# Kernel optimization log

Hardware: AMD Instinct MI355X
Metric: run time of the kernel (lower is better)

## Reference

```python
import jax, jax.numpy as jnp
import numpy as np

B, T, N = 512, 512, 128   # batch, timesteps, driving series
M = 64                    # LSTM hidden size
UNITS = 64                # attention units


def setup_inputs() -> dict:
    key = jax.random.key(0)
    ks = jax.random.split(key, 9)
    s = lambda fan_in: 1.0 / np.sqrt(fan_in)
    return {
        "x": jax.random.normal(ks[0], (B, T, N), jnp.float32),
        "hidden_state": jax.random.normal(ks[1], (B, M), jnp.float32),
        "cell_state": jax.random.normal(ks[2], (B, M), jnp.float32),
        # Dense(units) applied to x permuted to (B, N, T): kernel contracts T
        "w1_kernel": jax.random.normal(ks[3], (T, UNITS), jnp.float32) * s(T),
        "w1_bias": jnp.zeros((UNITS,), jnp.float32),
        # Dense(units) applied to query (B, N, 2M)
        "w2_kernel": jax.random.normal(ks[4], (2 * M, UNITS), jnp.float32) * s(2 * M),
        "w2_bias": jnp.zeros((UNITS,), jnp.float32),
        # Dense(1) scoring
        "v_kernel": jax.random.normal(ks[5], (UNITS, 1), jnp.float32) * s(UNITS),
        "v_bias": jnp.zeros((1,), jnp.float32),
    }


def reference(x, hidden_state, cell_state, w1_kernel, w1_bias,
              w2_kernel, w2_bias, v_kernel, v_bias):
    # query: (B, 2M) -> broadcast over the N feature axis (RepeatVector)
    query = jnp.concatenate([hidden_state, cell_state], axis=-1)
    q_proj = query @ w2_kernel + w2_bias                    # (B, UNITS)
    x_perm = jnp.transpose(x, (0, 2, 1))                    # (B, N, T)
    score = jnp.tanh(x_perm @ w1_kernel + w1_bias + q_proj[:, None, :])  # (B, N, UNITS)
    score = score @ v_kernel + v_bias                       # (B, N, 1)
    score = jnp.transpose(score, (0, 2, 1))                 # (B, 1, N)
    attention_weights = jax.nn.softmax(score, axis=-1)      # (B, 1, N)
    context_vector = jnp.sum(attention_weights * x, axis=-1)  # (B, T)
    return context_vector, attention_weights
```

## Files before the change

kernel.cpp:

```cpp
#include <hip/hip_runtime.h>
#include <hip/hip_bf16.h>

namespace {

constexpr int kB = 512, kT = 512, kN = 128, kM = 64, kU = 64;
constexpr int TT = 64;
constexpr int SX = 68;

typedef __attribute__((ext_vector_type(8))) short short8;
typedef __attribute__((ext_vector_type(16))) float f32x16;

__device__ __forceinline__ unsigned pack_hl(float v) {
  unsigned u = __float_as_uint(v);
  unsigned hs = (u + 0x7fffu + ((u >> 16) & 1u)) >> 16;
  float lo = v - __uint_as_float(hs << 16);
  unsigned ul = __float_as_uint(lo);
  unsigned ls = (ul + 0x7fffu + ((ul >> 16) & 1u)) >> 16;
  return (hs << 16) | (ls & 0xffffu);
}

__device__ __forceinline__ float fast_tanh(float x) {
  return 1.0f - 2.0f / (__expf(2.0f * x) + 1.0f);
}

union FragU { unsigned u[4]; short8 s; };

__device__ __forceinline__ void unpack_hl(const unsigned* p, short8& hi, short8& lo) {
  FragU H, L;
#pragma unroll
  for (int j = 0; j < 4; ++j) {
    unsigned a = p[2 * j], b = p[2 * j + 1];
    H.u[j] = (a >> 16) | (b & 0xffff0000u);
    L.u[j] = (a & 0xffffu) | (b << 16);
  }
  hi = H.s; lo = L.s;
}

struct __align__(16) SmemS {
  unsigned xsT[kN * SX];
  unsigned w1T[kU * SX];
  float qpart[8][kU];
  float sred[2][kN];
  float sn[kN];
};

__global__ __launch_bounds__(512, 4) void score_kernel(
    const float* __restrict__ x,
    const float* __restrict__ hs,
    const float* __restrict__ cs,
    const float* __restrict__ w1,
    const float* __restrict__ w1b,
    const float* __restrict__ w2,
    const float* __restrict__ w2b,
    const float* __restrict__ vk,
    float* __restrict__ aw_out)
{
  __shared__ SmemS s;
  const int b = blockIdx.x;
  const int tid = threadIdx.x;
  const int l = tid & 63;
  const int w = tid >> 6;

  {
    const int u = tid & 63, kg = tid >> 6;
    float a0 = 0.f;
#pragma unroll
    for (int j = 0; j < 16; ++j) {
      int k = kg * 16 + j;
      float qv = (k < kM) ? hs[(size_t)b * kM + k] : cs[(size_t)b * kM + (k - kM)];
      a0 = fmaf(qv, w2[k * kU + u], a0);
    }
    s.qpart[kg][u] = a0;
  }

  const int xn = l + 64 * (w & 1);
  const int xts = (w >> 1) * 16;
  const int wu = l;
  const int wts = w * 8;

  const int kh = l >> 5;
  const int mrow = (w & 3) * 32 + (l & 31);
  const int urow = (w >> 2) * 32 + (l & 31);

  f32x16 acc;
#pragma unroll
  for (int i = 0; i < 16; ++i) acc[i] = 0.f;

  float rx[16], rw[8];
#pragma unroll
  for (int j = 0; j < 16; ++j)
    rx[j] = x[((size_t)b * kT + xts + j) * kN + xn];
#pragma unroll
  for (int j = 0; j < 8; ++j)
    rw[j] = w1[(size_t)(wts + j) * kU + wu];

  for (int t0 = 0; t0 < kT; t0 += TT) {
    __syncthreads();
    {
      unsigned px[16];
#pragma unroll
      for (int j = 0; j < 16; ++j) px[j] = pack_hl(rx[j]);
#pragma unroll
      for (int jj = 0; jj < 4; ++jj)
        *(uint4*)&s.xsT[xn * SX + xts + 4 * jj] =
            make_uint4(px[4 * jj], px[4 * jj + 1], px[4 * jj + 2], px[4 * jj + 3]);
      unsigned pw[8];
#pragma unroll
      for (int j = 0; j < 8; ++j) pw[j] = pack_hl(rw[j]);
#pragma unroll
      for (int jj = 0; jj < 2; ++jj)
        *(uint4*)&s.w1T[wu * SX + wts + 4 * jj] =
            make_uint4(pw[4 * jj], pw[4 * jj + 1], pw[4 * jj + 2], pw[4 * jj + 3]);
    }
    __syncthreads();
    if (t0 + TT < kT) {
#pragma unroll
      for (int j = 0; j < 16; ++j)
        rx[j] = x[((size_t)b * kT + t0 + TT + xts + j) * kN + xn];
#pragma unroll
      for (int j = 0; j < 8; ++j)
        rw[j] = w1[(size_t)(t0 + TT + wts + j) * kU + wu];
    }

#pragma unroll
    for (int ss = 0; ss < 4; ++ss) {
      unsigned ra[8];
      const unsigned* pa = &s.xsT[mrow * SX + 16 * ss + 8 * kh];
      *(uint4*)&ra[0] = *(const uint4*)pa;
      *(uint4*)&ra[4] = *(const uint4*)(pa + 4);
      short8 ah, al;
      unpack_hl(ra, ah, al);

      unsigned rb[8];
      const unsigned* pb = &s.w1T[urow * SX + 16 * ss + 8 * kh];
      *(uint4*)&rb[0] = *(const uint4*)pb;
      *(uint4*)&rb[4] = *(const uint4*)(pb + 4);
      short8 bh, bl;
      unpack_hl(rb, bh, bl);

      acc = __builtin_amdgcn_mfma_f32_32x32x16_bf16(ah, bh, acc, 0, 0, 0);
      acc = __builtin_amdgcn_mfma_f32_32x32x16_bf16(ah, bl, acc, 0, 0, 0);
      acc = __builtin_amdgcn_mfma_f32_32x32x16_bf16(al, bh, acc, 0, 0, 0);
    }
  }

  float qpu = w2b[urow] + w1b[urow];
#pragma unroll
  for (int g = 0; g < 8; ++g) qpu += s.qpart[g][urow];
  const float vu = vk[urow];

  float pr[16];
#pragma unroll
  for (int r = 0; r < 16; ++r)
    pr[r] = fast_tanh(acc[r] + qpu) * vu;
#pragma unroll
  for (int off = 1; off < 32; off <<= 1)
#pragma unroll
    for (int r = 0; r < 16; ++r)
      pr[r] += __shfl_xor(pr[r], off);

  if ((l & 31) == 0) {
#pragma unroll
    for (int r = 0; r < 16; ++r)
      s.sred[w >> 2][(w & 3) * 32 + (r & 3) + 8 * (r >> 2) + 4 * kh] = pr[r];
  }
  __syncthreads();
  if (tid < kN) s.sn[tid] = s.sred[0][tid] + s.sred[1][tid];
  __syncthreads();

  if (tid < 64) {
    float s0 = s.sn[tid], s1 = s.sn[tid + 64];
    float m = fmaxf(s0, s1);
#pragma unroll
    for (int off = 32; off > 0; off >>= 1) m = fmaxf(m, __shfl_xor(m, off));
    float e0 = __expf(s0 - m), e1 = __expf(s1 - m);
    float se = e0 + e1;
#pragma unroll
    for (int off = 32; off > 0; off >>= 1) se += __shfl_xor(se, off);
    float inv = 1.0f / se;
    aw_out[(size_t)b * kN + tid] = e0 * inv;
    aw_out[(size_t)b * kN + tid + 64] = e1 * inv;
  }
}

__global__ __launch_bounds__(256) void context_kernel(
    const float* __restrict__ x,
    const float* __restrict__ aw_in,
    float* __restrict__ ctx)
{
  __shared__ float aw[kN];
  const int b = blockIdx.x >> 2;
  const int seg = blockIdx.x & 3;
  if (threadIdx.x < kN) aw[threadIdx.x] = aw_in[(size_t)b * kN + threadIdx.x];
  __syncthreads();

  const int lr = threadIdx.x & 3;
  const int row = threadIdx.x >> 2;
#pragma unroll
  for (int rg = 0; rg < 2; ++rg) {
    const int r = seg * 128 + rg * 64 + row;
    const float4* xp = (const float4*)(x + ((size_t)b * kT + r) * kN);
    float a = 0.f;
#pragma unroll
    for (int k = 0; k < 8; ++k) {
      int i = lr + k * 4;
      float4 v = xp[i];
      const float* wa = &aw[i * 4];
      a = fmaf(v.x, wa[0], a);
      a = fmaf(v.y, wa[1], a);
      a = fmaf(v.z, wa[2], a);
      a = fmaf(v.w, wa[3], a);
    }
    a += __shfl_xor(a, 1);
    a += __shfl_xor(a, 2);
    if (lr == 0) ctx[(size_t)b * kT + r] = a;
  }
}

}

extern "C" void kernel_launch(void* const* d_in, const int* in_sizes, int n_in,
                              void* d_out, int out_size, void* d_ws, size_t ws_size,
                              hipStream_t stream) {
  const float* x   = (const float*)d_in[0];
  const float* hs  = (const float*)d_in[1];
  const float* cs  = (const float*)d_in[2];
  const float* w1  = (const float*)d_in[3];
  const float* w1b = (const float*)d_in[4];
  const float* w2  = (const float*)d_in[5];
  const float* w2b = (const float*)d_in[6];
  const float* vk  = (const float*)d_in[7];

  float* out = (float*)d_out;
  float* ctx = out;
  float* awo = out + (size_t)kB * kT;

  hipLaunchKernelGGL(score_kernel, dim3(kB), dim3(512), 0, stream,
                     x, hs, cs, w1, w1b, w2, w2b, vk, awo);
  hipLaunchKernelGGL(context_kernel, dim3(kB * 4), dim3(256), 0, stream,
                     x, awo, ctx);
}
```

Baseline: 228.1 us.

## Fuse score and context kernels, keeping x in LDS as bf16

Merges the score and context kernels into one launch. Each block keeps its whole x slab in LDS as bf16 and reuses it for the context reduction, so x is read from global memory only once instead of twice. The T dimension is split across two wave groups, each producing full 64-unit accumulators, with an LDS reduction between them; w1 staging now uses a swizzled layout. The cost is very large dynamic LDS use, which limits occupancy, and the context is computed from bf16-rounded x, which lowers accuracy.

```diff
diff --git a/kernel.cpp b/kernel.cpp
--- a/kernel.cpp
+++ b/kernel.cpp
@@ -4,19 +4,24 @@
 namespace {
 
 constexpr int kB = 512, kT = 512, kN = 128, kM = 64, kU = 64;
-constexpr int TT = 64;
-constexpr int SX = 68;
+constexpr int WST = 72;
+constexpr int XST = 520;
+constexpr int RST = 12;
+constexpr int CST = 528;
 
 typedef __attribute__((ext_vector_type(8))) short short8;
 typedef __attribute__((ext_vector_type(16))) float f32x16;
 
+__device__ __forceinline__ unsigned rne16(float v) {
+  unsigned u = __float_as_uint(v);
+  return (u + 0x7fffu + ((u >> 16) & 1u)) >> 16;
+}
+__device__ __forceinline__ float fb16(unsigned h) { return __uint_as_float(h << 16); }
+
 __device__ __forceinline__ unsigned pack_hl(float v) {
-  unsigned u = __float_as_uint(v);
-  unsigned hs = (u + 0x7fffu + ((u >> 16) & 1u)) >> 16;
-  float lo = v - __uint_as_float(hs << 16);
-  unsigned ul = __float_as_uint(lo);
-  unsigned ls = (ul + 0x7fffu + ((ul >> 16) & 1u)) >> 16;
-  return (hs << 16) | (ls & 0xffffu);
+  unsigned h = rne16(v);
+  unsigned l = rne16(v - fb16(h));
+  return (h << 16) | (l & 0xffffu);
 }
 
 __device__ __forceinline__ float fast_tanh(float x) {
@@ -36,15 +41,33 @@
   hi = H.s; lo = L.s;
 }
 
-struct __align__(16) SmemS {
-  unsigned xsT[kN * SX];
-  unsigned w1T[kU * SX];
+__device__ __forceinline__ void pack8(const float* v, short8& hi, short8& lo) {
+  FragU H, L;
+#pragma unroll
+  for (int jj = 0; jj < 4; ++jj) {
+    float v0 = v[2 * jj], v1 = v[2 * jj + 1];
+    unsigned h0 = rne16(v0), h1 = rne16(v1);
+    unsigned l0 = rne16(v0 - fb16(h0)), l1 = rne16(v1 - fb16(h1));
+    H.u[jj] = h0 | (h1 << 16);
+    L.u[jj] = l0 | (l1 << 16);
+  }
+  hi = H.s; lo = L.s;
+}
+
+struct Smem {
+  union {
+    unsigned wstage[kU * WST];
+    float red[256 * RST];
+    float red2[8 * CST];
+  } u;
+  unsigned short xbf[kN * XST];
   float qpart[8][kU];
-  float sred[2][kN];
+  float qpfull[kU];
   float sn[kN];
+  float aw[kN];
 };
 
-__global__ __launch_bounds__(512, 4) void score_kernel(
+__global__ __launch_bounds__(512, 2) void fused_kernel(
     const float* __restrict__ x,
     const float* __restrict__ hs,
     const float* __restrict__ cs,
@@ -53,13 +76,21 @@
     const float* __restrict__ w2,
     const float* __restrict__ w2b,
     const float* __restrict__ vk,
+    float* __restrict__ ctx_out,
     float* __restrict__ aw_out)
 {
-  __shared__ SmemS s;
+  extern __shared__ char smem_raw[];
+  Smem& s = *reinterpret_cast<Smem*>(smem_raw);
+
   const int b = blockIdx.x;
   const int tid = threadIdx.x;
   const int l = tid & 63;
   const int w = tid >> 6;
+  const int g = w >> 2;
+  const int m = w & 3;
+  const int ln = l & 31;
+  const int kh = l >> 5;
+  const int nA = 32 * m + ln;
 
   {
     const int u = tid & 63, kg = tid >> 6;
@@ -73,147 +104,145 @@
     s.qpart[kg][u] = a0;
   }
 
-  const int xn = l + 64 * (w & 1);
-  const int xts = (w >> 1) * 16;
-  const int wu = l;
-  const int wts = w * 8;
-
-  const int kh = l >> 5;
-  const int mrow = (w & 3) * 32 + (l & 31);
-  const int urow = (w >> 2) * 32 + (l & 31);
-
-  f32x16 acc;
-#pragma unroll
-  for (int i = 0; i < 16; ++i) acc[i] = 0.f;
-
-  float rx[16], rw[8];
-#pragma unroll
-  for (int j = 0; j < 16; ++j)
-    rx[j] = x[((size_t)b * kT + xts + j) * kN + xn];
-#pragma unroll
-  for (int j = 0; j < 8; ++j)
-    rw[j] = w1[(size_t)(wts + j) * kU + wu];
-
-  for (int t0 = 0; t0 < kT; t0 += TT) {
-    __syncthreads();
-    {
-      unsigned px[16];
-#pragma unroll
-      for (int j = 0; j < 16; ++j) px[j] = pack_hl(rx[j]);
-#pragma unroll
-      for (int jj = 0; jj < 4; ++jj)
-        *(uint4*)&s.xsT[xn * SX + xts + 4 * jj] =
-            make_uint4(px[4 * jj], px[4 * jj + 1], px[4 * jj + 2], px[4 * jj + 3]);
-      unsigned pw[8];
-#pragma unroll
-      for (int j = 0; j < 8; ++j) pw[j] = pack_hl(rw[j]);
-#pragma unroll
-      for (int jj = 0; jj < 2; ++jj)
-        *(uint4*)&s.w1T[wu * SX + wts + 4 * jj] =
-            make_uint4(pw[4 * jj], pw[4 * jj + 1], pw[4 * jj + 2], pw[4 * jj + 3]);
-    }
-    __syncthreads();
-    if (t0 + TT < kT) {
-#pragma unroll
-      for (int j = 0; j < 16; ++j)
-        rx[j] = x[((size_t)b * kT + t0 + TT + xts + j) * kN + xn];
+  f32x16 acc0, acc1;
+#pragma unroll
+  for (int i = 0; i < 16; ++i) { acc0[i] = 0.f; acc1[i] = 0.f; }
+
+  for (int sub = 0; sub < 8; ++sub) {
+    const int tb = g * 256 + sub * 32;
+    __syncthreads();
+
+    float rA[2][8];
+#pragma unroll
+    for (int ks = 0; ks < 2; ++ks)
 #pragma unroll
       for (int j = 0; j < 8; ++j)
-        rw[j] = w1[(size_t)(t0 + TT + wts + j) * kU + wu];
-    }
-
-#pragma unroll
-    for (int ss = 0; ss < 4; ++ss) {
-      unsigned ra[8];
-      const unsigned* pa = &s.xsT[mrow * SX + 16 * ss + 8 * kh];
-      *(uint4*)&ra[0] = *(const uint4*)pa;
-      *(uint4*)&ra[4] = *(const uint4*)(pa + 4);
+        rA[ks][j] = x[((size_t)b * kT + tb + ks * 16 + 8 * kh + j) * kN + nA];
+
+#pragma unroll
+    for (int i = 0; i < 8; ++i) {
+      int idx = tid + i * 512;
+      int u = idx & 63, tr = idx >> 6;
+      int gg = tr >> 5, lt = tr & 31;
+      float v = w1[(size_t)(gg * 256 + sub * 32 + lt) * kU + u];
+      s.u.wstage[u * WST + 36 * gg + (lt ^ ((u & 7) << 2))] = pack_hl(v);
+    }
+    __syncthreads();
+
+#pragma unroll
+    for (int ks = 0; ks < 2; ++ks) {
       short8 ah, al;
-      unpack_hl(ra, ah, al);
-
-      unsigned rb[8];
-      const unsigned* pb = &s.w1T[urow * SX + 16 * ss + 8 * kh];
-      *(uint4*)&rb[0] = *(const uint4*)pb;
-      *(uint4*)&rb[4] = *(const uint4*)(pb + 4);
-      short8 bh, bl;
-      unpack_hl(rb, bh, bl);
-
-      acc = __builtin_amdgcn_mfma_f32_32x32x16_bf16(ah, bh, acc, 0, 0, 0);
-      acc = __builtin_amdgcn_mfma_f32_32x32x16_bf16(ah, bl, acc, 0, 0, 0);
-      acc = __builtin_amdgcn_mfma_f32_32x32x16_bf16(al, bh, acc, 0, 0, 0);
-    }
-  }
-
-  float qpu = w2b[urow] + w1b[urow];
-#pragma unroll
-  for (int g = 0; g < 8; ++g) qpu += s.qpart[g][urow];
-  const float vu = vk[urow];
-
-  float pr[16];
-#pragma unroll
-  for (int r = 0; r < 16; ++r)
-    pr[r] = fast_tanh(acc[r] + qpu) * vu;
-#pragma unroll
-  for (int off = 1; off < 32; off <<= 1)
+      pack8(rA[ks], ah, al);
+      const int tcur = tb + ks * 16 + 8 * kh;
+      *(short8*)&s.xbf[nA * XST + tcur] = ah;
+      const int ltk = ks * 16 + 8 * kh;
+#pragma unroll
+      for (int ut = 0; ut < 2; ++ut) {
+        const int u = 32 * ut + ln;
+        const int sw = (u & 7) << 2;
+        const unsigned* base = &s.u.wstage[u * WST + 36 * g];
+        unsigned rb[8];
+        *(uint4*)&rb[0] = *(const uint4*)&base[ltk ^ sw];
+        *(uint4*)&rb[4] = *(const uint4*)&base[(ltk + 4) ^ sw];
+        short8 bh, bl;
+        unpack_hl(rb, bh, bl);
+        f32x16& a = ut ? acc1 : acc0;
+        a = __builtin_amdgcn_mfma_f32_32x32x16_bf16(ah, bh, a, 0, 0, 0);
+        a = __builtin_amdgcn_mfma_f32_32x32x16_bf16(ah, bl, a, 0, 0, 0);
+        a = __builtin_amdgcn_mfma_f32_32x32x16_bf16(al, bh, a, 0, 0, 0);
+      }
+    }
+  }
+  __syncthreads();
+
+  const int rrow = ((w & 3) * 64 + l) * RST;
+#pragma unroll
+  for (int rnd = 0; rnd < 4; ++rnd) {
+    f32x16& a = (rnd < 2) ? acc0 : acc1;
+    const int off = (rnd & 1) * 8;
+    if (g == 1) {
+#pragma unroll
+      for (int j = 0; j < 8; ++j) s.u.red[rrow + j] = a[off + j];
+    }
+    __syncthreads();
+    if (g == 0) {
+#pragma unroll
+      for (int j = 0; j < 8; ++j) a[off + j] += s.u.red[rrow + j];
+    }
+    __syncthreads();
+  }
+
+  if (tid < kU) {
+    float v = w2b[tid] + w1b[tid];
+#pragma unroll
+    for (int gg = 0; gg < 8; ++gg) v += s.qpart[gg][tid];
+    s.qpfull[tid] = v;
+  }
+  __syncthreads();
+
+  if (g == 0) {
+    const float qp0 = s.qpfull[ln], qp1 = s.qpfull[32 + ln];
+    const float v0 = vk[ln], v1 = vk[32 + ln];
+    float pr[16];
 #pragma unroll
     for (int r = 0; r < 16; ++r)
-      pr[r] += __shfl_xor(pr[r], off);
-
-  if ((l & 31) == 0) {
-#pragma unroll
-    for (int r = 0; r < 16; ++r)
-      s.sred[w >> 2][(w & 3) * 32 + (r & 3) + 8 * (r >> 2) + 4 * kh] = pr[r];
-  }
-  __syncthreads();
-  if (tid < kN) s.sn[tid] = s.sred[0][tid] + s.sred[1][tid];
+      pr[r] = fmaf(fast_tanh(acc0[r] + qp0), v0, fast_tanh(acc1[r] + qp1) * v1);
+#pragma unroll
+    for (int off = 1; off < 32; off <<= 1)
+#pragma unroll
+      for (int r = 0; r < 16; ++r)
+        pr[r] += __shfl_xor(pr[r], off);
+    if (ln == 0) {
+#pragma unroll
+      for (int r = 0; r < 16; ++r)
+        s.sn[32 * m + (r & 3) + 8 * (r >> 2) + 4 * kh] = pr[r];
+    }
+  }
   __syncthreads();
 
   if (tid < 64) {
     float s0 = s.sn[tid], s1 = s.sn[tid + 64];
-    float m = fmaxf(s0, s1);
-#pragma unroll
-    for (int off = 32; off > 0; off >>= 1) m = fmaxf(m, __shfl_xor(m, off));
-    float e0 = __expf(s0 - m), e1 = __expf(s1 - m);
+    float mx = fmaxf(s0, s1);
+#pragma unroll
+    for (int off = 32; off > 0; off >>= 1) mx = fmaxf(mx, __shfl_xor(mx, off));
+    float e0 = __expf(s0 - mx), e1 = __expf(s1 - mx);
     float se = e0 + e1;
 #pragma unroll
     for (int off = 32; off > 0; off >>= 1) se += __shfl_xor(se, off);
     float inv = 1.0f / se;
-    aw_out[(size_t)b * kN + tid] = e0 * inv;
-    aw_out[(size_t)b * kN + tid + 64] = e1 * inv;
-  }
-}
-
-__global__ __launch_bounds__(256) void context_kernel(
-    const float* __restrict__ x,
-    const float* __restrict__ aw_in,
-    float* __restrict__ ctx)
-{
-  __shared__ float aw[kN];
-  const int b = blockIdx.x >> 2;
-  const int seg = blockIdx.x & 3;
-  if (threadIdx.x < kN) aw[threadIdx.x] = aw_in[(size_t)b * kN + threadIdx.x];
-  __syncthreads();
-
-  const int lr = threadIdx.x & 3;
-  const int row = threadIdx.x >> 2;
-#pragma unroll
-  for (int rg = 0; rg < 2; ++rg) {
-    const int r = seg * 128 + rg * 64 + row;
-    const float4* xp = (const float4*)(x + ((size_t)b * kT + r) * kN);
-    float a = 0.f;
-#pragma unroll
-    for (int k = 0; k < 8; ++k) {
-      int i = lr + k * 4;
-      float4 v = xp[i];
-      const float* wa = &aw[i * 4];
-      a = fmaf(v.x, wa[0], a);
-      a = fmaf(v.y, wa[1], a);
-      a = fmaf(v.z, wa[2], a);
-      a = fmaf(v.w, wa[3], a);
-    }
-    a += __shfl_xor(a, 1);
-    a += __shfl_xor(a, 2);
-    if (lr == 0) ctx[(size_t)b * kT + r] = a;
+    float a0 = e0 * inv, a1 = e1 * inv;
+    s.aw[tid] = a0;
+    s.aw[tid + 64] = a1;
+    aw_out[(size_t)b * kN + tid] = a0;
+    aw_out[(size_t)b * kN + tid + 64] = a1;
+  }
+  __syncthreads();
+
+  {
+    float cp[8];
+#pragma unroll
+    for (int j = 0; j < 8; ++j) cp[j] = 0.f;
+    const int nb = 16 * w;
+#pragma unroll
+    for (int nn = 0; nn < 16; ++nn) {
+      const int n = nb + nn;
+      const float a = s.aw[n];
+      short8 xv = *(const short8*)&s.xbf[n * XST + 8 * l];
+#pragma unroll
+      for (int j = 0; j < 8; ++j)
+        cp[j] = fmaf(fb16((unsigned)(unsigned short)xv[j]), a, cp[j]);
+    }
+    float4 c0 = {cp[0], cp[1], cp[2], cp[3]};
+    float4 c1 = {cp[4], cp[5], cp[6], cp[7]};
+    *(float4*)&s.u.red2[w * CST + 8 * l] = c0;
+    *(float4*)&s.u.red2[w * CST + 8 * l + 4] = c1;
+  }
+  __syncthreads();
+  {
+    float c = 0.f;
+#pragma unroll
+    for (int ww = 0; ww < 8; ++ww) c += s.u.red2[ww * CST + tid];
+    ctx_out[(size_t)b * kT + tid] = c;
   }
 }
 
@@ -235,8 +264,10 @@
   float* ctx = out;
   float* awo = out + (size_t)kB * kT;
 
-  hipLaunchKernelGGL(score_kernel, dim3(kB), dim3(512), 0, stream,
-                     x, hs, cs, w1, w1b, w2, w2b, vk, awo);
-  hipLaunchKernelGGL(context_kernel, dim3(kB * 4), dim3(256), 0, stream,
-                     x, awo, ctx);
-}
+  static_assert(sizeof(Smem) <= 160 * 1024, "LDS overflow");
+  (void)hipFuncSetAttribute(reinterpret_cast<const void*>(fused_kernel),
+                            hipFuncAttributeMaxDynamicSharedMemorySize,
+                            (int)sizeof(Smem));
+  hipLaunchKernelGGL(fused_kernel, dim3(kB), dim3(512), sizeof(Smem), stream,
+                     x, hs, cs, w1, w1b, w2, w2b, vk, ctx, awo);
+}
```

Result: faster. 222.0 us (-2.7%).

## Split score kernel across N halves and load x fragments directly into MFMA operands

Applied to the files above, without the earlier changes.

The score kernel now launches two 256-thread blocks per batch, each covering 64 of the 128 series. It drops the register prefetch and shared-memory staging of x; each lane reads its x fragment straight from global memory and packs it into hi/lo bf16 in registers. Raw scores go to a workspace, and the softmax moves into the context kernel, where every segment block recomputes it and only segment 0 writes the weights. This aims to raise parallelism and cut LDS use and barriers. The costs are strided, uncoalesced global reads of x with no prefetch overlap, and w1 staging plus the query projection now done twice per batch.

```diff
diff --git a/kernel.cpp b/kernel.cpp
--- a/kernel.cpp
+++ b/kernel.cpp
@@ -4,19 +4,21 @@
 namespace {
 
 constexpr int kB = 512, kT = 512, kN = 128, kM = 64, kU = 64;
-constexpr int TT = 64;
-constexpr int SX = 68;
+constexpr int WST = 68;
 
 typedef __attribute__((ext_vector_type(8))) short short8;
 typedef __attribute__((ext_vector_type(16))) float f32x16;
 
+__device__ __forceinline__ unsigned rne16(float v) {
+  unsigned u = __float_as_uint(v);
+  return (u + 0x7fffu + ((u >> 16) & 1u)) >> 16;
+}
+__device__ __forceinline__ float fb16(unsigned h) { return __uint_as_float(h << 16); }
+
 __device__ __forceinline__ unsigned pack_hl(float v) {
-  unsigned u = __float_as_uint(v);
-  unsigned hs = (u + 0x7fffu + ((u >> 16) & 1u)) >> 16;
-  float lo = v - __uint_as_float(hs << 16);
-  unsigned ul = __float_as_uint(lo);
-  unsigned ls = (ul + 0x7fffu + ((ul >> 16) & 1u)) >> 16;
-  return (hs << 16) | (ls & 0xffffu);
+  unsigned h = rne16(v);
+  unsigned l = rne16(v - fb16(h));
+  return (h << 16) | (l & 0xffffu);
 }
 
 __device__ __forceinline__ float fast_tanh(float x) {
@@ -36,15 +38,20 @@
   hi = H.s; lo = L.s;
 }
 
-struct __align__(16) SmemS {
-  unsigned xsT[kN * SX];
-  unsigned w1T[kU * SX];
-  float qpart[8][kU];
-  float sred[2][kN];
-  float sn[kN];
-};
-
-__global__ __launch_bounds__(512, 4) void score_kernel(
+__device__ __forceinline__ void pack8(const float* v, short8& hi, short8& lo) {
+  FragU H, L;
+#pragma unroll
+  for (int jj = 0; jj < 4; ++jj) {
+    float v0 = v[2 * jj], v1 = v[2 * jj + 1];
+    unsigned h0 = rne16(v0), h1 = rne16(v1);
+    unsigned l0 = rne16(v0 - fb16(h0)), l1 = rne16(v1 - fb16(h1));
+    H.u[jj] = h0 | (h1 << 16);
+    L.u[jj] = l0 | (l1 << 16);
+  }
+  hi = H.s; lo = L.s;
+}
+
+__global__ __launch_bounds__(256, 4) void score_kernel(
     const float* __restrict__ x,
     const float* __restrict__ hs,
     const float* __restrict__ cs,
@@ -53,86 +60,69 @@
     const float* __restrict__ w2,
     const float* __restrict__ w2b,
     const float* __restrict__ vk,
-    float* __restrict__ aw_out)
+    float* __restrict__ sn_out)
 {
-  __shared__ SmemS s;
-  const int b = blockIdx.x;
+  __shared__ unsigned wst[kU * WST];
+  __shared__ float qpart[4][kU];
+  __shared__ float qpfull[kU];
+  __shared__ float sred[2][kU];
+
+  const int bh = blockIdx.x;
+  const int b = bh >> 1;
+  const int h = bh & 1;
   const int tid = threadIdx.x;
   const int l = tid & 63;
   const int w = tid >> 6;
+  const int ln = l & 31;
+  const int kh = l >> 5;
+  const int m = w & 1;
+  const int ug = w >> 1;
+  const int nA = 64 * h + 32 * m + ln;
+  const int u = 32 * ug + ln;
 
   {
-    const int u = tid & 63, kg = tid >> 6;
+    const int uu = tid & 63, kg = tid >> 6;
     float a0 = 0.f;
 #pragma unroll
-    for (int j = 0; j < 16; ++j) {
-      int k = kg * 16 + j;
+    for (int j = 0; j < 32; ++j) {
+      int k = kg * 32 + j;
       float qv = (k < kM) ? hs[(size_t)b * kM + k] : cs[(size_t)b * kM + (k - kM)];
-      a0 = fmaf(qv, w2[k * kU + u], a0);
-    }
-    s.qpart[kg][u] = a0;
-  }
-
-  const int xn = l + 64 * (w & 1);
-  const int xts = (w >> 1) * 16;
-  const int wu = l;
-  const int wts = w * 8;
-
-  const int kh = l >> 5;
-  const int mrow = (w & 3) * 32 + (l & 31);
-  const int urow = (w >> 2) * 32 + (l & 31);
+      a0 = fmaf(qv, w2[k * kU + uu], a0);
+    }
+    qpart[kg][uu] = a0;
+  }
 
   f32x16 acc;
 #pragma unroll
   for (int i = 0; i < 16; ++i) acc[i] = 0.f;
 
-  float rx[16], rw[8];
-#pragma unroll
-  for (int j = 0; j < 16; ++j)
-    rx[j] = x[((size_t)b * kT + xts + j) * kN + xn];
-#pragma unroll
-  for (int j = 0; j < 8; ++j)
-    rw[j] = w1[(size_t)(wts + j) * kU + wu];
-
-  for (int t0 = 0; t0 < kT; t0 += TT) {
+  for (int tc = 0; tc < kT; tc += 64) {
     __syncthreads();
     {
-      unsigned px[16];
-#pragma unroll
-      for (int j = 0; j < 16; ++j) px[j] = pack_hl(rx[j]);
+      const int row = tid & 63;
+      const int cb = (tid >> 6) * 16;
+      unsigned pw[16];
+#pragma unroll
+      for (int j = 0; j < 16; ++j)
+        pw[j] = pack_hl(w1[(size_t)(tc + cb + j) * kU + row]);
 #pragma unroll
       for (int jj = 0; jj < 4; ++jj)
-        *(uint4*)&s.xsT[xn * SX + xts + 4 * jj] =
-            make_uint4(px[4 * jj], px[4 * jj + 1], px[4 * jj + 2], px[4 * jj + 3]);
-      unsigned pw[8];
-#pragma unroll
-      for (int j = 0; j < 8; ++j) pw[j] = pack_hl(rw[j]);
-#pragma unroll
-      for (int jj = 0; jj < 2; ++jj)
-        *(uint4*)&s.w1T[wu * SX + wts + 4 * jj] =
+        *(uint4*)&wst[row * WST + cb + 4 * jj] =
             make_uint4(pw[4 * jj], pw[4 * jj + 1], pw[4 * jj + 2], pw[4 * jj + 3]);
     }
     __syncthreads();
-    if (t0 + TT < kT) {
-#pragma unroll
-      for (int j = 0; j < 16; ++j)
-        rx[j] = x[((size_t)b * kT + t0 + TT + xts + j) * kN + xn];
+
+#pragma unroll
+    for (int ss = 0; ss < 4; ++ss) {
+      float rA[8];
 #pragma unroll
       for (int j = 0; j < 8; ++j)
-        rw[j] = w1[(size_t)(t0 + TT + wts + j) * kU + wu];
-    }
-
-#pragma unroll
-    for (int ss = 0; ss < 4; ++ss) {
-      unsigned ra[8];
-      const unsigned* pa = &s.xsT[mrow * SX + 16 * ss + 8 * kh];
-      *(uint4*)&ra[0] = *(const uint4*)pa;
-      *(uint4*)&ra[4] = *(const uint4*)(pa + 4);
+        rA[j] = x[((size_t)b * kT + tc + 16 * ss + 8 * kh + j) * kN + nA];
       short8 ah, al;
-      unpack_hl(ra, ah, al);
+      pack8(rA, ah, al);
 
       unsigned rb[8];
-      const unsigned* pb = &s.w1T[urow * SX + 16 * ss + 8 * kh];
+      const unsigned* pb = &wst[u * WST + 16 * ss + 8 * kh];
       *(uint4*)&rb[0] = *(const uint4*)pb;
       *(uint4*)&rb[4] = *(const uint4*)(pb + 4);
       short8 bh, bl;
@@ -143,55 +133,70 @@
       acc = __builtin_amdgcn_mfma_f32_32x32x16_bf16(al, bh, acc, 0, 0, 0);
     }
   }
-
-  float qpu = w2b[urow] + w1b[urow];
-#pragma unroll
-  for (int g = 0; g < 8; ++g) qpu += s.qpart[g][urow];
-  const float vu = vk[urow];
-
-  float pr[16];
-#pragma unroll
-  for (int r = 0; r < 16; ++r)
-    pr[r] = fast_tanh(acc[r] + qpu) * vu;
-#pragma unroll
-  for (int off = 1; off < 32; off <<= 1)
+  __syncthreads();
+
+  if (tid < kU) {
+    float v = w2b[tid] + w1b[tid];
+#pragma unroll
+    for (int g = 0; g < 4; ++g) v += qpart[g][tid];
+    qpfull[tid] = v;
+  }
+  __syncthreads();
+
+  {
+    const float qp = qpfull[u];
+    const float vu = vk[u];
+    float pr[16];
 #pragma unroll
     for (int r = 0; r < 16; ++r)
-      pr[r] += __shfl_xor(pr[r], off);
-
-  if ((l & 31) == 0) {
-#pragma unroll
-    for (int r = 0; r < 16; ++r)
-      s.sred[w >> 2][(w & 3) * 32 + (r & 3) + 8 * (r >> 2) + 4 * kh] = pr[r];
-  }
-  __syncthreads();
-  if (tid < kN) s.sn[tid] = s.sred[0][tid] + s.sred[1][tid];
-  __syncthreads();
-
-  if (tid < 64) {
-    float s0 = s.sn[tid], s1 = s.sn[tid + 64];
-    float m = fmaxf(s0, s1);
-#pragma unroll
-    for (int off = 32; off > 0; off >>= 1) m = fmaxf(m, __shfl_xor(m, off));
-    float e0 = __expf(s0 - m), e1 = __expf(s1 - m);
-    float se = e0 + e1;
-#pragma unroll
-    for (int off = 32; off > 0; off >>= 1) se += __shfl_xor(se, off);
-    float inv = 1.0f / se;
-    aw_out[(size_t)b * kN + tid] = e0 * inv;
-    aw_out[(size_t)b * kN + tid + 64] = e1 * inv;
-  }
+      pr[r] = fast_tanh(acc[r] + qp) * vu;
+#pragma unroll
+    for (int off = 1; off < 32; off <<= 1)
+#pragma unroll
+      for (int r = 0; r < 16; ++r)
+        pr[r] += __shfl_xor(pr[r], off);
+    if (ln == 0) {
+#pragma unroll
+      for (int r = 0; r < 16; ++r)
+        sred[ug][32 * m + (r & 3) + 8 * (r >> 2) + 4 * kh] = pr[r];
+    }
+  }
+  __syncthreads();
+  if (tid < 64)
+    sn_out[(size_t)b * kN + 64 * h + tid] = sred[0][tid] + sred[1][tid];
 }
 
 __global__ __launch_bounds__(256) void context_kernel(
     const float* __restrict__ x,
-    const float* __restrict__ aw_in,
-    float* __restrict__ ctx)
+    const float* __restrict__ sn_in,
+    float* __restrict__ ctx,
+    float* __restrict__ aw_out)
 {
+  __shared__ float sm[kN];
   __shared__ float aw[kN];
   const int b = blockIdx.x >> 2;
   const int seg = blockIdx.x & 3;
-  if (threadIdx.x < kN) aw[threadIdx.x] = aw_in[(size_t)b * kN + threadIdx.x];
+  if (threadIdx.x < kN) sm[threadIdx.x] = sn_in[(size_t)b * kN + threadIdx.x];
+  __syncthreads();
+
+  if (threadIdx.x < 64) {
+    float s0 = sm[threadIdx.x], s1 = sm[threadIdx.x + 64];
+    float mx = fmaxf(s0, s1);
+#pragma unroll
+    for (int off = 32; off > 0; off >>= 1) mx = fmaxf(mx, __shfl_xor(mx, off));
+    float e0 = __expf(s0 - mx), e1 = __expf(s1 - mx);
+    float se = e0 + e1;
+#pragma unroll
+    for (int off = 32; off > 0; off >>= 1) se += __shfl_xor(se, off);
+    float inv = 1.0f / se;
+    float a0 = e0 * inv, a1 = e1 * inv;
+    aw[threadIdx.x] = a0;
+    aw[threadIdx.x + 64] = a1;
+    if (seg == 0) {
+      aw_out[(size_t)b * kN + threadIdx.x] = a0;
+      aw_out[(size_t)b * kN + threadIdx.x + 64] = a1;
+    }
+  }
   __syncthreads();
 
   const int lr = threadIdx.x & 3;
@@ -234,9 +239,10 @@
   float* out = (float*)d_out;
   float* ctx = out;
   float* awo = out + (size_t)kB * kT;
-
-  hipLaunchKernelGGL(score_kernel, dim3(kB), dim3(512), 0, stream,
-                     x, hs, cs, w1, w1b, w2, w2b, vk, awo);
+  float* sn  = (float*)d_ws;
+
+  hipLaunchKernelGGL(score_kernel, dim3(kB * 2), dim3(256), 0, stream,
+                     x, hs, cs, w1, w1b, w2, w2b, vk, sn);
   hipLaunchKernelGGL(context_kernel, dim3(kB * 4), dim3(256), 0, stream,
-                     x, awo, ctx);
-}
+                     x, sn, ctx, awo);
+}
```

Result: slower. 232.7 us (+2.0%).
